# Kernel tuning notes

Hardware: AMD Instinct MI355X
Metric: run time of the kernel (lower is better)

The kernel has to match this reference:

```python
import jax, jax.numpy as jnp
import numpy as np
import math

B, S, HID, NH, K_SIG = 8, 8192, 1024, 16, 1024
HD = HID // NH
SCALE = math.sqrt(HD)

def _lin(x, W, b):
    # torch nn.Linear: x @ W.T + b, W is [out, in]
    return jnp.einsum('...i,oi->...o', x, W) + b

def setup_inputs() -> dict:
    key = jax.random.key(0)
    ks = jax.random.split(key, 16)
    hidden_states = jax.random.normal(ks[0], (B, S, HID), jnp.float32)
    # mask with exactly K_SIG ones per row (matches torch padding semantics exactly)
    perm = jax.vmap(lambda k: jax.random.permutation(k, S))(jax.random.split(ks[1], B))
    idx = perm[:, :K_SIG]
    mask = jnp.zeros((B, S), bool).at[jnp.arange(B)[:, None], idx].set(True)
    register_state = jax.random.normal(ks[2], (B, HID), jnp.float32)
    def w(k):
        return jax.random.normal(k, (HID, HID), jnp.float32) * 0.02
    def bvec(k):
        return jax.random.normal(k, (HID,), jnp.float32) * 0.02
    return {
        'hidden_states': hidden_states, 'mask': mask, 'register_state': register_state,
        'Wq': w(ks[3]), 'bq': bvec(ks[4]), 'Wk': w(ks[5]), 'bk': bvec(ks[6]),
        'Wv': w(ks[7]), 'bv': bvec(ks[8]), 'Wo': w(ks[9]), 'bo': bvec(ks[10]),
        'Wrk': w(ks[11]), 'brk': bvec(ks[12]), 'Wrv': w(ks[13]), 'brv': bvec(ks[14]),
    }

def reference(hidden_states, mask, register_state, Wq, bq, Wk, bk, Wv, bv, Wo, bo, Wrk, brk, Wrv, brv):
    # sorted indices of the K_SIG True positions per row (stable argsort puts
    # True (~mask == False) first, in original order)
    idx = jnp.argsort(jnp.logical_not(mask), axis=1, stable=True)[:, :K_SIG]  # [B, K_SIG]
    signal = jnp.take_along_axis(hidden_states, idx[:, :, None], axis=1)      # [B, K_SIG, HID]

    Q = _lin(signal, Wq, bq).reshape(B, K_SIG, NH, HD)
    Kt = _lin(signal, Wk, bk)
    Vt = _lin(signal, Wv, bv)
    Kr = _lin(register_state, Wrk, brk)[:, None, :]
    Vr = _lin(register_state, Wrv, brv)[:, None, :]
    K = jnp.concatenate([Kt, Kr], axis=1).reshape(B, K_SIG + 1, NH, HD)
    V = jnp.concatenate([Vt, Vr], axis=1).reshape(B, K_SIG + 1, NH, HD)

    scores = jnp.einsum('bqhd,bkhd->bhqk', Q, K) / SCALE
    attn = jax.nn.softmax(scores, axis=-1)
    ao = jnp.einsum('bhqk,bkhd->bqhd', attn, V).reshape(B, K_SIG, HID)
    ao = _lin(ao, Wo, bo)

    # scatter back into a copy of hidden_states
    out = hidden_states.at[jnp.arange(B)[:, None], idx].set(ao)
    return out
```

## Files before the change

### kernel.cpp

```cpp
#include <hip/hip_runtime.h>
#include <hip/hip_bf16.h>
#include <math.h>

#define Bc    8
#define Sc    8192
#define HIDc  1024
#define NHc   16
#define HDc   64
#define KSc   1024
#define QSCALE 0.18033688f

typedef __bf16 bf16_t;
typedef __bf16 bf16x8 __attribute__((ext_vector_type(8)));
typedef float  f32x4  __attribute__((ext_vector_type(4)));

#define OFF_FLAG  ((size_t)0)
#define OFF_IDX   ((size_t)256)
#define OFF_INV   ((size_t)33024)
#define OFF_SIG   ((size_t)295168)
#define OFF_WQKV  ((size_t)17072384)
#define OFF_WO    ((size_t)23363840)
#define OFF_QKV   ((size_t)25460992)
#define OFF_KR    ((size_t)75792640)
#define OFF_VR    ((size_t)75809024)
#define OFF_AO    ((size_t)75825408)

__device__ inline void gll16(const bf16_t* g, bf16_t* l) {
  __builtin_amdgcn_global_load_lds(
      (const __attribute__((address_space(1))) void*)g,
      (__attribute__((address_space(3))) void*)l, 16, 0, 0);
}

__global__ void build_idx_kernel(const unsigned char* m8, int* flag,
                                 int* idx, int* inv) {
  __shared__ int cnt[256];
  __shared__ int f_sh;
  int b = blockIdx.x, t = threadIdx.x;
  const unsigned char* raw = m8 + (size_t)b * Sc;
  int c8 = 0;
  for (int i = t; i < Sc; i += 256) c8 += (raw[i] != 0);
  cnt[t] = c8;
  __syncthreads();
  for (int s2 = 128; s2 > 0; s2 >>= 1) {
    if (t < s2) cnt[t] += cnt[t + s2];
    __syncthreads();
  }
  if (t == 0) {
    f_sh = (cnt[0] == KSc) ? 1 : 0;
    if (b == 0) *flag = f_sh;
  }
  __syncthreads();
  const int f = f_sh;
  const int* m32 = (const int*)m8;
  int base = b * Sc + t * 32;
  int c = 0;
  for (int i = 0; i < 32; i++)
    c += f ? (m8[base + i] != 0) : (m32[base + i] != 0);
  cnt[t] = c;
  __syncthreads();
  if (t == 0) {
    int run = 0;
    for (int j = 0; j < 256; j++) { int v = cnt[j]; cnt[j] = run; run += v; }
  }
  __syncthreads();
  int off = b * KSc + cnt[t];
  for (int i = 0; i < 32; i++) {
    int on = f ? (m8[base + i] != 0) : (m32[base + i] != 0);
    if (on) { idx[off] = t * 32 + i; inv[base + i] = off; off++; }
  }
}

__global__ __launch_bounds__(256) void copy_gather_kernel(
    const float* __restrict__ hidden, const unsigned char* __restrict__ m8,
    const int* __restrict__ flag, const int* __restrict__ inv,
    float* __restrict__ dout, bf16_t* __restrict__ sig) {
  const int f = *flag;
  const int* m32 = (const int*)m8;
  const int t = threadIdx.x;
  const int row0 = blockIdx.x * 32;
  for (int i = 0; i < 32; i++) {
    const int row = row0 + i;
    const int on = f ? (m8[row] != 0) : (m32[row] != 0);
    const float4 v = *(const float4*)(hidden + (size_t)row * HIDc + t * 4);
    if (on) {
      bf16_t* d = sig + (size_t)inv[row] * HIDc + t * 4;
      d[0] = (bf16_t)v.x; d[1] = (bf16_t)v.y; d[2] = (bf16_t)v.z; d[3] = (bf16_t)v.w;
    } else {
      *(float4*)(dout + (size_t)row * HIDc + t * 4) = v;
    }
  }
}

__global__ __launch_bounds__(256) void prep_kernel(
    const float* __restrict__ Wq, const float* __restrict__ Wk,
    const float* __restrict__ Wv, const float* __restrict__ Wo,
    const float* __restrict__ rst,
    const float* __restrict__ Wrk, const float* __restrict__ brk,
    const float* __restrict__ Wrv, const float* __restrict__ brv,
    bf16_t* __restrict__ Wqkv, bf16_t* __restrict__ Wob,
    bf16_t* __restrict__ Krb, bf16_t* __restrict__ Vrb) {
  const int bid = blockIdx.x;
  if (bid < 4096) {
    int gid = bid * 256 + threadIdx.x;
    int e4 = gid * 4;
    if (e4 < 3 * 1048576) {
      int sel = e4 >> 20, cc = e4 & 1048575;
      const float* src = sel == 0 ? Wq : (sel == 1 ? Wk : Wv);
      float4 v = *(const float4*)(src + cc);
      bf16_t* d = Wqkv + e4;
      d[0] = (bf16_t)v.x; d[1] = (bf16_t)v.y; d[2] = (bf16_t)v.z; d[3] = (bf16_t)v.w;
    } else {
      int cc = e4 - 3 * 1048576;
      float4 v = *(const float4*)(Wo + cc);
      bf16_t* d = Wob + cc;
      d[0] = (bf16_t)v.x; d[1] = (bf16_t)v.y; d[2] = (bf16_t)v.z; d[3] = (bf16_t)v.w;
    }
  } else {
    const int wid = (bid - 4096) * 4 + (threadIdx.x >> 6);
    const int lane = threadIdx.x & 63;
    const int isV = wid >> 10, j = wid & 1023;
    const float* Wrow = (isV ? Wrv : Wrk) + (size_t)j * HIDc;
    float4 w[4];
#pragma unroll
    for (int i = 0; i < 4; i++) w[i] = ((const float4*)Wrow)[i * 64 + lane];
    const float bias = (isV ? brv : brk)[j];
#pragma unroll
    for (int b = 0; b < 8; b++) {
      const float4* r4 = (const float4*)(rst + (size_t)b * HIDc);
      float s = 0.f;
#pragma unroll
      for (int i = 0; i < 4; i++) {
        float4 r = r4[i * 64 + lane];
        s += w[i].x * r.x + w[i].y * r.y + w[i].z * r.z + w[i].w * r.w;
      }
      s += __shfl_xor(s, 1);  s += __shfl_xor(s, 2);  s += __shfl_xor(s, 4);
      s += __shfl_xor(s, 8);  s += __shfl_xor(s, 16); s += __shfl_xor(s, 32);
      if (lane == 0)
        (isV ? Vrb : Krb)[(size_t)b * HIDc + j] = (bf16_t)(s + bias);
    }
  }
}

__device__ inline void gemm_mainloop(const bf16_t* __restrict__ A,
                                     const bf16_t* __restrict__ Bw,
                                     int tile_m, int tile_n,
                                     bf16_t* As, bf16_t* Bs, f32x4 acc[4][4]) {
  const int t = threadIdx.x, lane = t & 63, w = t >> 6;
  const int wm = w >> 1, wn = w & 1;
  const int r16 = lane & 15, kq = lane >> 4;
  for (int k0 = 0; k0 < 1024; k0 += 32) {
#pragma unroll
    for (int rr = 0; rr < 2; ++rr) {
      int e = rr * 2048 + w * 512 + lane * 8;
      int row = e >> 5, kk = e & 31;
      gll16(A + (size_t)(tile_m + row) * 1024 + k0 + kk, As + rr * 2048 + w * 512);
      gll16(Bw + (size_t)(tile_n + row) * 1024 + k0 + kk, Bs + rr * 2048 + w * 512);
    }
    __syncthreads();
    bf16x8 af[4], bfr[4];
#pragma unroll
    for (int m = 0; m < 4; m++)
      af[m] = *(const bf16x8*)(As + (wm * 64 + m * 16 + r16) * 32 + kq * 8);
#pragma unroll
    for (int n = 0; n < 4; n++)
      bfr[n] = *(const bf16x8*)(Bs + (wn * 64 + n * 16 + r16) * 32 + kq * 8);
#pragma unroll
    for (int m = 0; m < 4; m++)
#pragma unroll
      for (int n = 0; n < 4; n++)
        acc[m][n] = __builtin_amdgcn_mfma_f32_16x16x32_bf16(af[m], bfr[n], acc[m][n], 0, 0, 0);
    __syncthreads();
  }
}

__global__ __launch_bounds__(256) void gemm_qkv_kernel(
    const bf16_t* __restrict__ A, const bf16_t* __restrict__ Bw,
    const float* __restrict__ bq, const float* __restrict__ bk,
    const float* __restrict__ bv, bf16_t* __restrict__ C) {
  __shared__ bf16_t As[128 * 32];
  __shared__ bf16_t Bs[128 * 32];
  const int tile_m = blockIdx.y * 128, tile_n = blockIdx.x * 128;
  f32x4 acc[4][4] = {};
  gemm_mainloop(A, Bw, tile_m, tile_n, As, Bs, acc);
  const int t = threadIdx.x, lane = t & 63, w = t >> 6;
  const int wm = w >> 1, wn = w & 1;
  const int r16 = lane & 15, kq = lane >> 4;
#pragma unroll
  for (int m = 0; m < 4; m++)
#pragma unroll
    for (int n = 0; n < 4; n++) {
      int col = tile_n + wn * 64 + n * 16 + r16;
      int sel = col >> 10, cc = col & 1023;
      float bias = sel == 0 ? bq[cc] : (sel == 1 ? bk[cc] : bv[cc]);
#pragma unroll
      for (int r = 0; r < 4; r++) {
        int row = tile_m + wm * 64 + m * 16 + kq * 4 + r;
        float v = acc[m][n][r] + bias;
        if (sel == 0) v *= QSCALE;
        C[(size_t)row * 3072 + col] = (bf16_t)v;
      }
    }
}

__global__ __launch_bounds__(256) void gemm_ao_kernel(
    const bf16_t* __restrict__ A, const bf16_t* __restrict__ Bw,
    const float* __restrict__ bo, const int* __restrict__ idx,
    float* __restrict__ dout) {
  __shared__ bf16_t As[128 * 32];
  __shared__ bf16_t Bs[128 * 32];
  const int tile_m = blockIdx.y * 128, tile_n = blockIdx.x * 128;
  f32x4 acc[4][4] = {};
  gemm_mainloop(A, Bw, tile_m, tile_n, As, Bs, acc);
  const int t = threadIdx.x, lane = t & 63, w = t >> 6;
  const int wm = w >> 1, wn = w & 1;
  const int r16 = lane & 15, kq = lane >> 4;
#pragma unroll
  for (int m = 0; m < 4; m++)
#pragma unroll
    for (int n = 0; n < 4; n++) {
      int col = tile_n + wn * 64 + n * 16 + r16;
      float bias = bo[col];
#pragma unroll
      for (int r = 0; r < 4; r++) {
        int row = tile_m + wm * 64 + m * 16 + kq * 4 + r;
        float v = acc[m][n][r] + bias;
        int bb = row >> 10;
        int drow = idx[row];
        dout[((size_t)bb * Sc + drow) * HIDc + col] = v;
      }
    }
}

__global__ __launch_bounds__(512) void attn_kernel(
    const bf16_t* __restrict__ QKV, const bf16_t* __restrict__ Krb,
    const bf16_t* __restrict__ Vrb, bf16_t* __restrict__ AO) {
  __shared__ bf16_t Kb[3][4096];
  __shared__ bf16_t Vt[2][4096];
  __shared__ bf16_t Pl[8][2048];
  const int t = threadIdx.x, lane = t & 63, w = t >> 6;
  const int gbk = blockIdx.x;
  const int li = (gbk & 7) * 64 + (gbk >> 3);
  const int qt = li & 3, h = (li >> 2) & 15, b = li >> 6;
  const int r16 = lane & 15, kq = lane >> 4;
  const int qbase = qt * 256 + w * 32;

  const int kK = t >> 3;
  const int dK = ((t & 7) ^ (kK & 7)) * 8;
  const bf16_t* kSrc = QKV + (size_t)(b * KSc + kK) * 3072 + 1024 + h * 64 + dK;
  const int kv8 = t >> 3, dv8 = (t & 7) * 8;
  const int vchunk = kv8 >> 3, voff = kv8 & 7, t7 = t & 7;
  const bf16_t* vSrc = QKV + (size_t)(b * KSc + kv8) * 3072 + 2048 + h * 64 + dv8;

  bf16x8 qf[2][2];
#pragma unroll
  for (int m = 0; m < 2; m++)
#pragma unroll
    for (int kc = 0; kc < 2; kc++)
      qf[m][kc] = *(const bf16x8*)(QKV +
          (size_t)(b * KSc + qbase + m * 16 + r16) * 3072 + h * 64 + kc * 32 + kq * 8);

  f32x4 o[2][4] = {};
  f32x4 osum[2] = {};

  bf16x8 vones;
#pragma unroll
  for (int j = 0; j < 8; j++) vones[j] = (bf16_t)1.0f;

  {
    bf16x8 v0 = *(const bf16x8*)vSrc;
    gll16(kSrc, &Kb[0][w * 512]);
    gll16(kSrc + (size_t)64 * 3072, &Kb[1][w * 512]);
#pragma unroll
    for (int j = 0; j < 8; j++)
      Vt[0][(dv8 + j) * 64 + (((vchunk ^ j ^ t7) << 3) | voff)] = v0[j];
  }
  asm volatile("s_waitcnt vmcnt(1) lgkmcnt(0)" ::: "memory");
  __builtin_amdgcn_s_barrier();

  for (int kt = 0; kt < 17; ++kt) {
    const int cbK = kt % 3;
    const int cbV = kt & 1, nbV = cbV ^ 1;
    bf16x8 vreg = {};
    if (kt < 15) {
      vreg = *(const bf16x8*)(vSrc + (size_t)(kt + 1) * 64 * 3072);
    } else if (kt == 15) {
      if (kv8 == 0) vreg = *(const bf16x8*)(Vrb + (size_t)b * HIDc + h * 64 + dv8);
    }
    if (kt <= 13) {
      gll16(kSrc + (size_t)(kt + 2) * 64 * 3072, &Kb[(kt + 2) % 3][w * 512]);
    } else if (kt == 14) {
      bf16x8 kz = {};
      if (kK == 0) kz = *(const bf16x8*)(Krb + (size_t)b * HIDc + h * 64 + dK);
      *(bf16x8*)(&Kb[1][t * 8]) = kz;
    }
    const bf16_t* Ks = Kb[cbK];

    f32x4 s[2][4] = {};
    __builtin_amdgcn_s_setprio(1);
#pragma unroll
    for (int n = 0; n < 4; n++) {
      const int rowk = n * 16 + r16;
#pragma unroll
      for (int kc = 0; kc < 2; kc++) {
        bf16x8 kf = *(const bf16x8*)(Ks + rowk * 64 +
                                     (((kc * 4 + kq) ^ (rowk & 7)) << 3));
#pragma unroll
        for (int m = 0; m < 2; m++)
          s[m][n] = __builtin_amdgcn_mfma_f32_16x16x32_bf16(kf, qf[m][kc], s[m][n], 0, 0, 0);
      }
    }
    __builtin_amdgcn_s_setprio(0);

    if (kt == 16) {
#pragma unroll
      for (int m = 0; m < 2; m++)
#pragma unroll
        for (int n = 0; n < 4; n++)
#pragma unroll
          for (int r = 0; r < 4; r++)
            if (!(n == 0 && kq == 0 && r == 0)) s[m][n][r] = -1e30f;
    }

    bf16_t* Pw = Pl[w];
#pragma unroll
    for (int m = 0; m < 2; m++)
#pragma unroll
      for (int n = 0; n < 4; n++) {
        float p0 = exp2f(s[m][n][0]), p1 = exp2f(s[m][n][1]);
        float p2 = exp2f(s[m][n][2]), p3 = exp2f(s[m][n][3]);
        unsigned lo, hi;
        asm("v_cvt_pk_bf16_f32 %0, %1, %2" : "=v"(lo) : "v"(p0), "v"(p1));
        asm("v_cvt_pk_bf16_f32 %0, %1, %2" : "=v"(hi) : "v"(p2), "v"(p3));
        unsigned long long pk = (unsigned long long)lo |
                                ((unsigned long long)hi << 32);
        *(unsigned long long*)(Pw + (m * 16 + r16) * 64 +
                               ((n * 16 + kq * 4) ^ ((r16 & 7) << 3))) = pk;
      }

    bf16x8 pa[2][2];
#pragma unroll
    for (int m = 0; m < 2; m++)
#pragma unroll
      for (int kc = 0; kc < 2; kc++)
        pa[m][kc] = *(const bf16x8*)(Pw + (m * 16 + r16) * 64 +
                                     ((kc * 32 + kq * 8) ^ ((r16 & 7) << 3)));

    const bf16_t* Vrow = Vt[cbV];
    __builtin_amdgcn_s_setprio(1);
#pragma unroll
    for (int n = 0; n < 4; n++) {
      const int rowv = n * 16 + r16;
      const int xr = (r16 & 7) ^ ((2 * n + (r16 >> 3)) & 7);
#pragma unroll
      for (int kc = 0; kc < 2; kc++) {
        bf16x8 vb = *(const bf16x8*)(Vrow + rowv * 64 +
                                     (((kc * 4 + kq) ^ xr) << 3));
#pragma unroll
        for (int m = 0; m < 2; m++)
          o[m][n] = __builtin_amdgcn_mfma_f32_16x16x32_bf16(pa[m][kc], vb, o[m][n], 0, 0, 0);
      }
    }
#pragma unroll
    for (int m = 0; m < 2; m++)
#pragma unroll
      for (int kc = 0; kc < 2; kc++)
        osum[m] = __builtin_amdgcn_mfma_f32_16x16x32_bf16(pa[m][kc], vones, osum[m], 0, 0, 0);
    __builtin_amdgcn_s_setprio(0);

    if (kt < 16) {
#pragma unroll
      for (int j = 0; j < 8; j++)
        Vt[nbV][(dv8 + j) * 64 + (((vchunk ^ j ^ t7) << 3) | voff)] = vreg[j];
      asm volatile("s_waitcnt vmcnt(1) lgkmcnt(0)" ::: "memory");
      __builtin_amdgcn_s_barrier();
    }
  }

#pragma unroll
  for (int m = 0; m < 2; m++)
#pragma unroll
    for (int n = 0; n < 4; n++)
#pragma unroll
      for (int r = 0; r < 4; r++) {
        float v = o[m][n][r] / osum[m][r];
        int rowg = b * KSc + qbase + m * 16 + kq * 4 + r;
        int col = h * 64 + n * 16 + r16;
        AO[(size_t)rowg * HIDc + col] = (bf16_t)v;
      }
}

extern "C" void kernel_launch(void* const* d_in, const int* in_sizes, int n_in,
                              void* d_out, int out_size, void* d_ws, size_t ws_size,
                              hipStream_t stream) {
  const float* hidden = (const float*)d_in[0];
  const void*  maskp  = d_in[1];
  const float* rst    = (const float*)d_in[2];
  const float* Wq = (const float*)d_in[3];  const float* bq = (const float*)d_in[4];
  const float* Wk = (const float*)d_in[5];  const float* bk = (const float*)d_in[6];
  const float* Wv = (const float*)d_in[7];  const float* bv = (const float*)d_in[8];
  const float* Wo = (const float*)d_in[9];  const float* bo = (const float*)d_in[10];
  const float* Wrk = (const float*)d_in[11]; const float* brk = (const float*)d_in[12];
  const float* Wrv = (const float*)d_in[13]; const float* brv = (const float*)d_in[14];
  float* dout = (float*)d_out;

  char* ws = (char*)d_ws;
  int*    flag = (int*)(ws + OFF_FLAG);
  int*    idx  = (int*)(ws + OFF_IDX);
  int*    inv  = (int*)(ws + OFF_INV);
  bf16_t* sig  = (bf16_t*)(ws + OFF_SIG);
  bf16_t* Wqkv = (bf16_t*)(ws + OFF_WQKV);
  bf16_t* Wob  = (bf16_t*)(ws + OFF_WO);
  bf16_t* QKV  = (bf16_t*)(ws + OFF_QKV);
  bf16_t* Krb  = (bf16_t*)(ws + OFF_KR);
  bf16_t* Vrb  = (bf16_t*)(ws + OFF_VR);
  bf16_t* AO   = (bf16_t*)(ws + OFF_AO);

  build_idx_kernel<<<Bc, 256, 0, stream>>>((const unsigned char*)maskp, flag, idx, inv);
  copy_gather_kernel<<<2048, 256, 0, stream>>>(hidden, (const unsigned char*)maskp,
                                               flag, inv, dout, sig);
  prep_kernel<<<4608, 256, 0, stream>>>(Wq, Wk, Wv, Wo, rst, Wrk, brk, Wrv, brv,
                                        Wqkv, Wob, Krb, Vrb);
  gemm_qkv_kernel<<<dim3(24, 64), 256, 0, stream>>>(sig, Wqkv, bq, bk, bv, QKV);
  attn_kernel<<<512, 512, 0, stream>>>(QKV, Krb, Vrb, AO);
  gemm_ao_kernel<<<dim3(8, 64), 256, 0, stream>>>(AO, Wob, bo, idx, dout);
}
```

Before: 315.4 us.

## Fuse index build, gather/copy, and weight prep into one front kernel

Merges the mask-index build, the hidden-state gather/copy and the weight conversion/register projection into a single launch. Each gather block now recomputes its own prefix count of the mask directly instead of relying on a precomputed inverse map, which removes two kernel launches and the serial dependency on the build_idx kernel. The trade-off is redundant mask scanning per block, up to 8K mask reads for the prefix plus a full 8K scan for the format flag. That extra scanning adds latency to the bandwidth-bound copy path.

After: 323.5 us. +2.6%, slower.

```diff
diff --git a/kernel.cpp b/kernel.cpp
--- a/kernel.cpp
+++ b/kernel.cpp
@@ -14,9 +14,7 @@
 typedef __bf16 bf16x8 __attribute__((ext_vector_type(8)));
 typedef float  f32x4  __attribute__((ext_vector_type(4)));
 
-#define OFF_FLAG  ((size_t)0)
 #define OFF_IDX   ((size_t)256)
-#define OFF_INV   ((size_t)33024)
 #define OFF_SIG   ((size_t)295168)
 #define OFF_WQKV  ((size_t)17072384)
 #define OFF_WO    ((size_t)23363840)
@@ -31,112 +29,136 @@
       (__attribute__((address_space(3))) void*)l, 16, 0, 0);
 }
 
-__global__ void build_idx_kernel(const unsigned char* m8, int* flag,
-                                 int* idx, int* inv) {
-  __shared__ int cnt[256];
-  __shared__ int f_sh;
-  int b = blockIdx.x, t = threadIdx.x;
-  const unsigned char* raw = m8 + (size_t)b * Sc;
-  int c8 = 0;
-  for (int i = t; i < Sc; i += 256) c8 += (raw[i] != 0);
-  cnt[t] = c8;
-  __syncthreads();
-  for (int s2 = 128; s2 > 0; s2 >>= 1) {
-    if (t < s2) cnt[t] += cnt[t + s2];
-    __syncthreads();
-  }
-  if (t == 0) {
-    f_sh = (cnt[0] == KSc) ? 1 : 0;
-    if (b == 0) *flag = f_sh;
-  }
-  __syncthreads();
-  const int f = f_sh;
-  const int* m32 = (const int*)m8;
-  int base = b * Sc + t * 32;
-  int c = 0;
-  for (int i = 0; i < 32; i++)
-    c += f ? (m8[base + i] != 0) : (m32[base + i] != 0);
-  cnt[t] = c;
-  __syncthreads();
-  if (t == 0) {
-    int run = 0;
-    for (int j = 0; j < 256; j++) { int v = cnt[j]; cnt[j] = run; run += v; }
-  }
-  __syncthreads();
-  int off = b * KSc + cnt[t];
-  for (int i = 0; i < 32; i++) {
-    int on = f ? (m8[base + i] != 0) : (m32[base + i] != 0);
-    if (on) { idx[off] = t * 32 + i; inv[base + i] = off; off++; }
-  }
-}
-
-__global__ __launch_bounds__(256) void copy_gather_kernel(
+__global__ __launch_bounds__(256) void front_kernel(
     const float* __restrict__ hidden, const unsigned char* __restrict__ m8,
-    const int* __restrict__ flag, const int* __restrict__ inv,
-    float* __restrict__ dout, bf16_t* __restrict__ sig) {
-  const int f = *flag;
-  const int* m32 = (const int*)m8;
-  const int t = threadIdx.x;
-  const int row0 = blockIdx.x * 32;
-  for (int i = 0; i < 32; i++) {
-    const int row = row0 + i;
-    const int on = f ? (m8[row] != 0) : (m32[row] != 0);
-    const float4 v = *(const float4*)(hidden + (size_t)row * HIDc + t * 4);
-    if (on) {
-      bf16_t* d = sig + (size_t)inv[row] * HIDc + t * 4;
-      d[0] = (bf16_t)v.x; d[1] = (bf16_t)v.y; d[2] = (bf16_t)v.z; d[3] = (bf16_t)v.w;
-    } else {
-      *(float4*)(dout + (size_t)row * HIDc + t * 4) = v;
-    }
-  }
-}
-
-__global__ __launch_bounds__(256) void prep_kernel(
     const float* __restrict__ Wq, const float* __restrict__ Wk,
     const float* __restrict__ Wv, const float* __restrict__ Wo,
     const float* __restrict__ rst,
     const float* __restrict__ Wrk, const float* __restrict__ brk,
     const float* __restrict__ Wrv, const float* __restrict__ brv,
+    float* __restrict__ dout, bf16_t* __restrict__ sig,
     bf16_t* __restrict__ Wqkv, bf16_t* __restrict__ Wob,
-    bf16_t* __restrict__ Krb, bf16_t* __restrict__ Vrb) {
-  const int bid = blockIdx.x;
-  if (bid < 4096) {
-    int gid = bid * 256 + threadIdx.x;
-    int e4 = gid * 4;
-    if (e4 < 3 * 1048576) {
-      int sel = e4 >> 20, cc = e4 & 1048575;
-      const float* src = sel == 0 ? Wq : (sel == 1 ? Wk : Wv);
-      float4 v = *(const float4*)(src + cc);
-      bf16_t* d = Wqkv + e4;
-      d[0] = (bf16_t)v.x; d[1] = (bf16_t)v.y; d[2] = (bf16_t)v.z; d[3] = (bf16_t)v.w;
+    bf16_t* __restrict__ Krb, bf16_t* __restrict__ Vrb,
+    int* __restrict__ idx) {
+  __shared__ int shc[256];
+  __shared__ int rowslot[32];
+  __shared__ int f_sh;
+  const int bid = blockIdx.x, t = threadIdx.x;
+
+  if (bid < 2048) {
+    const int b = bid >> 8;
+    const int lrow0 = (bid & 255) * 32;
+    int c = 0;
+    for (int i = t; i < 8192; i += 256) c += (m8[i] != 0);
+    shc[t] = c;
+    __syncthreads();
+    for (int s2 = 128; s2 > 0; s2 >>= 1) {
+      if (t < s2) shc[t] += shc[t + s2];
+      __syncthreads();
+    }
+    if (t == 0) f_sh = (shc[0] == KSc) ? 1 : 0;
+    __syncthreads();
+    const int f = f_sh;
+    const unsigned char* mb8 = m8 + (size_t)b * Sc;
+    const int* mb32 = (const int*)m8 + (size_t)b * Sc;
+    __syncthreads();
+    int c2 = 0;
+    for (int i = t; i < lrow0; i += 256) c2 += f ? (mb8[i] != 0) : (mb32[i] != 0);
+    shc[t] = c2;
+    __syncthreads();
+    for (int s2 = 128; s2 > 0; s2 >>= 1) {
+      if (t < s2) shc[t] += shc[t + s2];
+      __syncthreads();
+    }
+    if (t < 32) {
+      int extra = 0;
+      for (int i = 0; i < t; i++)
+        extra += f ? (mb8[lrow0 + i] != 0) : (mb32[lrow0 + i] != 0);
+      rowslot[t] = b * KSc + shc[0] + extra;
+    }
+    __syncthreads();
+    for (int i = 0; i < 32; i++) {
+      const int lrow = lrow0 + i;
+      const int on = f ? (mb8[lrow] != 0) : (mb32[lrow] != 0);
+      const float4 v = *(const float4*)(hidden + ((size_t)b * Sc + lrow) * HIDc + t * 4);
+      if (on) {
+        bf16_t* d = sig + (size_t)rowslot[i] * HIDc + t * 4;
+        d[0] = (bf16_t)v.x; d[1] = (bf16_t)v.y; d[2] = (bf16_t)v.z; d[3] = (bf16_t)v.w;
+      } else {
+        *(float4*)(dout + ((size_t)b * Sc + lrow) * HIDc + t * 4) = v;
+      }
+    }
+  } else if (bid < 6656) {
+    const int pb = bid - 2048;
+    if (pb < 4096) {
+      int gid = pb * 256 + t;
+      int e4 = gid * 4;
+      if (e4 < 3 * 1048576) {
+        int sel = e4 >> 20, cc = e4 & 1048575;
+        const float* src = sel == 0 ? Wq : (sel == 1 ? Wk : Wv);
+        float4 v = *(const float4*)(src + cc);
+        bf16_t* d = Wqkv + e4;
+        d[0] = (bf16_t)v.x; d[1] = (bf16_t)v.y; d[2] = (bf16_t)v.z; d[3] = (bf16_t)v.w;
+      } else {
+        int cc = e4 - 3 * 1048576;
+        float4 v = *(const float4*)(Wo + cc);
+        bf16_t* d = Wob + cc;
+        d[0] = (bf16_t)v.x; d[1] = (bf16_t)v.y; d[2] = (bf16_t)v.z; d[3] = (bf16_t)v.w;
+      }
     } else {
-      int cc = e4 - 3 * 1048576;
-      float4 v = *(const float4*)(Wo + cc);
-      bf16_t* d = Wob + cc;
-      d[0] = (bf16_t)v.x; d[1] = (bf16_t)v.y; d[2] = (bf16_t)v.z; d[3] = (bf16_t)v.w;
+      const int wid = (pb - 4096) * 4 + (t >> 6);
+      const int lane = t & 63;
+      const int isV = wid >> 10, j = wid & 1023;
+      const float* Wrow = (isV ? Wrv : Wrk) + (size_t)j * HIDc;
+      float4 w[4];
+#pragma unroll
+      for (int i = 0; i < 4; i++) w[i] = ((const float4*)Wrow)[i * 64 + lane];
+      const float bias = (isV ? brv : brk)[j];
+#pragma unroll
+      for (int b = 0; b < 8; b++) {
+        const float4* r4 = (const float4*)(rst + (size_t)b * HIDc);
+        float s = 0.f;
+#pragma unroll
+        for (int i = 0; i < 4; i++) {
+          float4 r = r4[i * 64 + lane];
+          s += w[i].x * r.x + w[i].y * r.y + w[i].z * r.z + w[i].w * r.w;
+        }
+        s += __shfl_xor(s, 1);  s += __shfl_xor(s, 2);  s += __shfl_xor(s, 4);
+        s += __shfl_xor(s, 8);  s += __shfl_xor(s, 16); s += __shfl_xor(s, 32);
+        if (lane == 0)
+          (isV ? Vrb : Krb)[(size_t)b * HIDc + j] = (bf16_t)(s + bias);
+      }
     }
   } else {
-    const int wid = (bid - 4096) * 4 + (threadIdx.x >> 6);
-    const int lane = threadIdx.x & 63;
-    const int isV = wid >> 10, j = wid & 1023;
-    const float* Wrow = (isV ? Wrv : Wrk) + (size_t)j * HIDc;
-    float4 w[4];
-#pragma unroll
-    for (int i = 0; i < 4; i++) w[i] = ((const float4*)Wrow)[i * 64 + lane];
-    const float bias = (isV ? brv : brk)[j];
-#pragma unroll
-    for (int b = 0; b < 8; b++) {
-      const float4* r4 = (const float4*)(rst + (size_t)b * HIDc);
-      float s = 0.f;
-#pragma unroll
-      for (int i = 0; i < 4; i++) {
-        float4 r = r4[i * 64 + lane];
-        s += w[i].x * r.x + w[i].y * r.y + w[i].z * r.z + w[i].w * r.w;
-      }
-      s += __shfl_xor(s, 1);  s += __shfl_xor(s, 2);  s += __shfl_xor(s, 4);
-      s += __shfl_xor(s, 8);  s += __shfl_xor(s, 16); s += __shfl_xor(s, 32);
-      if (lane == 0)
-        (isV ? Vrb : Krb)[(size_t)b * HIDc + j] = (bf16_t)(s + bias);
+    const int b = bid - 6656;
+    const unsigned char* raw = m8 + (size_t)b * Sc;
+    int c8 = 0;
+    for (int i = t; i < Sc; i += 256) c8 += (raw[i] != 0);
+    shc[t] = c8;
+    __syncthreads();
+    for (int s2 = 128; s2 > 0; s2 >>= 1) {
+      if (t < s2) shc[t] += shc[t + s2];
+      __syncthreads();
+    }
+    if (t == 0) f_sh = (shc[0] == KSc) ? 1 : 0;
+    __syncthreads();
+    const int f = f_sh;
+    const int* m32 = (const int*)m8;
+    int base = b * Sc + t * 32;
+    int c = 0;
+    for (int i = 0; i < 32; i++)
+      c += f ? (m8[base + i] != 0) : (m32[base + i] != 0);
+    shc[t] = c;
+    __syncthreads();
+    if (t == 0) {
+      int run = 0;
+      for (int j = 0; j < 256; j++) { int v = shc[j]; shc[j] = run; run += v; }
+    }
+    __syncthreads();
+    int off = b * KSc + shc[t];
+    for (int i = 0; i < 32; i++) {
+      int on = f ? (m8[base + i] != 0) : (m32[base + i] != 0);
+      if (on) { idx[off] = t * 32 + i; off++; }
     }
   }
 }
@@ -404,9 +426,7 @@
   float* dout = (float*)d_out;
 
   char* ws = (char*)d_ws;
-  int*    flag = (int*)(ws + OFF_FLAG);
   int*    idx  = (int*)(ws + OFF_IDX);
-  int*    inv  = (int*)(ws + OFF_INV);
   bf16_t* sig  = (bf16_t*)(ws + OFF_SIG);
   bf16_t* Wqkv = (bf16_t*)(ws + OFF_WQKV);
   bf16_t* Wob  = (bf16_t*)(ws + OFF_WO);
@@ -415,11 +435,9 @@
   bf16_t* Vrb  = (bf16_t*)(ws + OFF_VR);
   bf16_t* AO   = (bf16_t*)(ws + OFF_AO);
 
-  build_idx_kernel<<<Bc, 256, 0, stream>>>((const unsigned char*)maskp, flag, idx, inv);
-  copy_gather_kernel<<<2048, 256, 0, stream>>>(hidden, (const unsigned char*)maskp,
-                                               flag, inv, dout, sig);
-  prep_kernel<<<4608, 256, 0, stream>>>(Wq, Wk, Wv, Wo, rst, Wrk, brk, Wrv, brv,
-                                        Wqkv, Wob, Krb, Vrb);
+  front_kernel<<<6664, 256, 0, stream>>>(
+      hidden, (const unsigned char*)maskp, Wq, Wk, Wv, Wo, rst,
+      Wrk, brk, Wrv, brv, dout, sig, Wqkv, Wob, Krb, Vrb, idx);
   gemm_qkv_kernel<<<dim3(24, 64), 256, 0, stream>>>(sig, Wqkv, bq, bk, bv, QKV);
   attn_kernel<<<512, 512, 0, stream>>>(QKV, Krb, Vrb, AO);
   gemm_ao_kernel<<<dim3(8, 64), 256, 0, stream>>>(AO, Wob, bo, idx, dout);
```

## Overlap passthrough copy with QKV GEMM and fuse signal gather into weight prep

Applied to the files above, without the earlier changes.

The signal-row gather now happens inside the weight conversion kernel, indexed by idx, so only the selected rows are read there. The copy of unmasked rows to the output moves into the QKV GEMM launch, with the blocks interleaved 3 GEMM tiles to 4 copy chunks. The aim is to run the memory-bound copy of hidden_states concurrently with the compute-bound GEMM and to drop one launch. The cost is that the copy and the GEMM tiles now compete for memory bandwidth and CU slots. The flag buffer is gone, and inv now marks unmasked rows with -1.

New measurement: 440.4 us. 1.4x slower.

```diff
diff --git a/kernel.cpp b/kernel.cpp
--- a/kernel.cpp
+++ b/kernel.cpp
@@ -14,7 +14,6 @@
 typedef __bf16 bf16x8 __attribute__((ext_vector_type(8)));
 typedef float  f32x4  __attribute__((ext_vector_type(4)));
 
-#define OFF_FLAG  ((size_t)0)
 #define OFF_IDX   ((size_t)256)
 #define OFF_INV   ((size_t)33024)
 #define OFF_SIG   ((size_t)295168)
@@ -31,77 +30,72 @@
       (__attribute__((address_space(3))) void*)l, 16, 0, 0);
 }
 
-__global__ void build_idx_kernel(const unsigned char* m8, int* flag,
-                                 int* idx, int* inv) {
-  __shared__ int cnt[256];
+__global__ __launch_bounds__(256) void front1_kernel(
+    const unsigned char* __restrict__ m8, int* __restrict__ idx,
+    int* __restrict__ inv) {
+  __shared__ int shc[256];
   __shared__ int f_sh;
-  int b = blockIdx.x, t = threadIdx.x;
+  const int b = blockIdx.x, t = threadIdx.x;
   const unsigned char* raw = m8 + (size_t)b * Sc;
   int c8 = 0;
   for (int i = t; i < Sc; i += 256) c8 += (raw[i] != 0);
-  cnt[t] = c8;
+  shc[t] = c8;
   __syncthreads();
   for (int s2 = 128; s2 > 0; s2 >>= 1) {
-    if (t < s2) cnt[t] += cnt[t + s2];
+    if (t < s2) shc[t] += shc[t + s2];
     __syncthreads();
   }
-  if (t == 0) {
-    f_sh = (cnt[0] == KSc) ? 1 : 0;
-    if (b == 0) *flag = f_sh;
-  }
+  if (t == 0) f_sh = (shc[0] == KSc) ? 1 : 0;
   __syncthreads();
   const int f = f_sh;
   const int* m32 = (const int*)m8;
-  int base = b * Sc + t * 32;
+  const int base = b * Sc + t * 32;
   int c = 0;
   for (int i = 0; i < 32; i++)
     c += f ? (m8[base + i] != 0) : (m32[base + i] != 0);
-  cnt[t] = c;
+  shc[t] = c;
   __syncthreads();
   if (t == 0) {
     int run = 0;
-    for (int j = 0; j < 256; j++) { int v = cnt[j]; cnt[j] = run; run += v; }
+    for (int j = 0; j < 256; j++) { int v = shc[j]; shc[j] = run; run += v; }
   }
   __syncthreads();
-  int off = b * KSc + cnt[t];
+  int off = b * KSc + shc[t];
   for (int i = 0; i < 32; i++) {
     int on = f ? (m8[base + i] != 0) : (m32[base + i] != 0);
     if (on) { idx[off] = t * 32 + i; inv[base + i] = off; off++; }
-  }
-}
-
-__global__ __launch_bounds__(256) void copy_gather_kernel(
-    const float* __restrict__ hidden, const unsigned char* __restrict__ m8,
-    const int* __restrict__ flag, const int* __restrict__ inv,
-    float* __restrict__ dout, bf16_t* __restrict__ sig) {
-  const int f = *flag;
-  const int* m32 = (const int*)m8;
-  const int t = threadIdx.x;
-  const int row0 = blockIdx.x * 32;
-  for (int i = 0; i < 32; i++) {
-    const int row = row0 + i;
-    const int on = f ? (m8[row] != 0) : (m32[row] != 0);
-    const float4 v = *(const float4*)(hidden + (size_t)row * HIDc + t * 4);
-    if (on) {
-      bf16_t* d = sig + (size_t)inv[row] * HIDc + t * 4;
-      d[0] = (bf16_t)v.x; d[1] = (bf16_t)v.y; d[2] = (bf16_t)v.z; d[3] = (bf16_t)v.w;
-    } else {
-      *(float4*)(dout + (size_t)row * HIDc + t * 4) = v;
-    }
-  }
-}
-
-__global__ __launch_bounds__(256) void prep_kernel(
+    else    { inv[base + i] = -1; }
+  }
+}
+
+__global__ __launch_bounds__(256) void front2_kernel(
+    const float* __restrict__ hidden, const int* __restrict__ idx,
     const float* __restrict__ Wq, const float* __restrict__ Wk,
     const float* __restrict__ Wv, const float* __restrict__ Wo,
     const float* __restrict__ rst,
     const float* __restrict__ Wrk, const float* __restrict__ brk,
     const float* __restrict__ Wrv, const float* __restrict__ brv,
-    bf16_t* __restrict__ Wqkv, bf16_t* __restrict__ Wob,
-    bf16_t* __restrict__ Krb, bf16_t* __restrict__ Vrb) {
-  const int bid = blockIdx.x;
-  if (bid < 4096) {
-    int gid = bid * 256 + threadIdx.x;
+    bf16_t* __restrict__ sig, bf16_t* __restrict__ Wqkv,
+    bf16_t* __restrict__ Wob, bf16_t* __restrict__ Krb,
+    bf16_t* __restrict__ Vrb) {
+  const int bid = blockIdx.x, t = threadIdx.x;
+  if (bid < 1024) {
+    const int s0 = bid * 8;
+    const int b = s0 >> 10;
+    float4 v[8];
+#pragma unroll
+    for (int j = 0; j < 8; j++) {
+      const int srow = idx[s0 + j];
+      v[j] = *(const float4*)(hidden + ((size_t)b * Sc + srow) * HIDc + t * 4);
+    }
+#pragma unroll
+    for (int j = 0; j < 8; j++) {
+      bf16_t* d = sig + (size_t)(s0 + j) * HIDc + t * 4;
+      d[0] = (bf16_t)v[j].x; d[1] = (bf16_t)v[j].y;
+      d[2] = (bf16_t)v[j].z; d[3] = (bf16_t)v[j].w;
+    }
+  } else if (bid < 5120) {
+    int gid = (bid - 1024) * 256 + t;
     int e4 = gid * 4;
     if (e4 < 3 * 1048576) {
       int sel = e4 >> 20, cc = e4 & 1048575;
@@ -116,8 +110,8 @@
       d[0] = (bf16_t)v.x; d[1] = (bf16_t)v.y; d[2] = (bf16_t)v.z; d[3] = (bf16_t)v.w;
     }
   } else {
-    const int wid = (bid - 4096) * 4 + (threadIdx.x >> 6);
-    const int lane = threadIdx.x & 63;
+    const int wid = (bid - 5120) * 4 + (t >> 6);
+    const int lane = t & 63;
     const int isV = wid >> 10, j = wid & 1023;
     const float* Wrow = (isV ? Wrv : Wrk) + (size_t)j * HIDc;
     float4 w[4];
@@ -173,33 +167,59 @@
   }
 }
 
-__global__ __launch_bounds__(256) void gemm_qkv_kernel(
+__global__ __launch_bounds__(256) void qkv_copy_kernel(
     const bf16_t* __restrict__ A, const bf16_t* __restrict__ Bw,
     const float* __restrict__ bq, const float* __restrict__ bk,
-    const float* __restrict__ bv, bf16_t* __restrict__ C) {
+    const float* __restrict__ bv, bf16_t* __restrict__ C,
+    const float* __restrict__ hidden, const int* __restrict__ inv,
+    float* __restrict__ dout) {
   __shared__ bf16_t As[128 * 32];
   __shared__ bf16_t Bs[128 * 32];
-  const int tile_m = blockIdx.y * 128, tile_n = blockIdx.x * 128;
-  f32x4 acc[4][4] = {};
-  gemm_mainloop(A, Bw, tile_m, tile_n, As, Bs, acc);
-  const int t = threadIdx.x, lane = t & 63, w = t >> 6;
-  const int wm = w >> 1, wn = w & 1;
-  const int r16 = lane & 15, kq = lane >> 4;
-#pragma unroll
-  for (int m = 0; m < 4; m++)
-#pragma unroll
-    for (int n = 0; n < 4; n++) {
-      int col = tile_n + wn * 64 + n * 16 + r16;
-      int sel = col >> 10, cc = col & 1023;
-      float bias = sel == 0 ? bq[cc] : (sel == 1 ? bk[cc] : bv[cc]);
-#pragma unroll
-      for (int r = 0; r < 4; r++) {
-        int row = tile_m + wm * 64 + m * 16 + kq * 4 + r;
-        float v = acc[m][n][r] + bias;
-        if (sel == 0) v *= QSCALE;
-        C[(size_t)row * 3072 + col] = (bf16_t)v;
-      }
-    }
+  const int bid = blockIdx.x, t = threadIdx.x;
+  const int g7 = bid / 7, r7 = bid % 7;
+  if (r7 < 3) {
+    const int tile = g7 * 3 + r7;
+    const int tile_m = (tile / 24) * 128, tile_n = (tile % 24) * 128;
+    f32x4 acc[4][4] = {};
+    gemm_mainloop(A, Bw, tile_m, tile_n, As, Bs, acc);
+    const int lane = t & 63, w = t >> 6;
+    const int wm = w >> 1, wn = w & 1;
+    const int r16 = lane & 15, kq = lane >> 4;
+#pragma unroll
+    for (int m = 0; m < 4; m++)
+#pragma unroll
+      for (int n = 0; n < 4; n++) {
+        int col = tile_n + wn * 64 + n * 16 + r16;
+        int sel = col >> 10, cc = col & 1023;
+        float bias = sel == 0 ? bq[cc] : (sel == 1 ? bk[cc] : bv[cc]);
+#pragma unroll
+        for (int r = 0; r < 4; r++) {
+          int row = tile_m + wm * 64 + m * 16 + kq * 4 + r;
+          float v = acc[m][n][r] + bias;
+          if (sel == 0) v *= QSCALE;
+          C[(size_t)row * 3072 + col] = (bf16_t)v;
+        }
+      }
+  } else {
+    const int c = g7 * 4 + (r7 - 3);
+    const int row0 = c * 32;
+#pragma unroll 1
+    for (int g = 0; g < 4; g++) {
+      const int rbase = row0 + g * 8;
+      int iv[8];
+      float4 v[8];
+#pragma unroll
+      for (int j = 0; j < 8; j++) iv[j] = inv[rbase + j];
+#pragma unroll
+      for (int j = 0; j < 8; j++)
+        if (iv[j] < 0)
+          v[j] = *(const float4*)(hidden + (size_t)(rbase + j) * HIDc + t * 4);
+#pragma unroll
+      for (int j = 0; j < 8; j++)
+        if (iv[j] < 0)
+          *(float4*)(dout + (size_t)(rbase + j) * HIDc + t * 4) = v[j];
+    }
+  }
 }
 
 __global__ __launch_bounds__(256) void gemm_ao_kernel(
@@ -404,7 +424,6 @@
   float* dout = (float*)d_out;
 
   char* ws = (char*)d_ws;
-  int*    flag = (int*)(ws + OFF_FLAG);
   int*    idx  = (int*)(ws + OFF_IDX);
   int*    inv  = (int*)(ws + OFF_INV);
   bf16_t* sig  = (bf16_t*)(ws + OFF_SIG);
@@ -415,12 +434,12 @@
   bf16_t* Vrb  = (bf16_t*)(ws + OFF_VR);
   bf16_t* AO   = (bf16_t*)(ws + OFF_AO);
 
-  build_idx_kernel<<<Bc, 256, 0, stream>>>((const unsigned char*)maskp, flag, idx, inv);
-  copy_gather_kernel<<<2048, 256, 0, stream>>>(hidden, (const unsigned char*)maskp,
-                                               flag, inv, dout, sig);
-  prep_kernel<<<4608, 256, 0, stream>>>(Wq, Wk, Wv, Wo, rst, Wrk, brk, Wrv, brv,
-                                        Wqkv, Wob, Krb, Vrb);
-  gemm_qkv_kernel<<<dim3(24, 64), 256, 0, stream>>>(sig, Wqkv, bq, bk, bv, QKV);
+  front1_kernel<<<Bc, 256, 0, stream>>>((const unsigned char*)maskp, idx, inv);
+  front2_kernel<<<5632, 256, 0, stream>>>(hidden, idx, Wq, Wk, Wv, Wo, rst,
+                                          Wrk, brk, Wrv, brv,
+                                          sig, Wqkv, Wob, Krb, Vrb);
+  qkv_copy_kernel<<<3584, 256, 0, stream>>>(sig, Wqkv, bq, bk, bv, QKV,
+                                            hidden, inv, dout);
   attn_kernel<<<512, 512, 0, stream>>>(QKV, Krb, Vrb, AO);
   gemm_ao_kernel<<<dim3(8, 64), 256, 0, stream>>>(AO, Wob, bo, idx, dout);
 }
```
